# Performance work log

Hardware: AMD Instinct MI355X
Metric: run time of the kernel (lower is better)

The kernel has to match this reference:

```python
import jax, jax.numpy as jnp
import numpy as np

EPSILON = float(np.finfo(np.float32).tiny)
K = 32                 # self.k
TRAIN_ENSEMBLE = 2     # repeat_sample in train mode
TAU = 0.1


def setup_inputs() -> dict:
    key = jax.random.key(0)
    scores = jax.random.normal(key, (256, 8192, 4), dtype=jnp.float32)  # [bsz, Nmax, ensemble]
    return {"scores": scores}


def reference(scores):
    bsz, Nmax, ensemble = scores.shape
    repeat = TRAIN_ENSEMBLE
    local_k = min(K, Nmax)

    # flat_scores: (bsz*ensemble, Nmax), then repeated over samples -> (repeat*bsz*ensemble, Nmax)
    flat = scores.transpose(0, 2, 1).reshape(bsz * ensemble, Nmax)
    flat = jnp.tile(flat, (repeat, 1))

    # Gumbel(0,1) noise (m.sample())
    g = jax.random.gumbel(jax.random.key(42), flat.shape, dtype=flat.dtype)
    flat = flat + g

    zeros = jnp.zeros_like(flat)

    def step(carry, _):
        f, khot, onehot = carry
        khot_mask = jnp.maximum(1.0 - onehot, EPSILON)
        f = f + jnp.log(khot_mask)
        onehot = jax.nn.softmax(f / TAU, axis=1)
        return (f, khot + onehot, onehot), None

    (_, khot, _), _ = jax.lax.scan(step, (flat, zeros, zeros), None, length=local_k)

    # hard top-k straight-through
    _, ind = jax.lax.top_k(khot, local_k)                      # (R, local_k)
    rows = jnp.arange(khot.shape[0])[:, None]
    khot_hard = jnp.zeros_like(khot).at[rows, ind].set(1.0)
    res = khot_hard - jax.lax.stop_gradient(khot) + khot

    # (repeat, bsz, ensemble, Nmax) -> (repeat, bsz, Nmax, ensemble)
    new_mask = res.reshape(repeat, bsz, ensemble, Nmax).transpose(0, 1, 3, 2)
    return new_mask
```

## Files before the change

### kernel.cpp

```cpp
#include <hip/hip_runtime.h>

#define TPB 256
#define ROWN 8192
#define CMAX 1024
#define EPS_TINY 1.1754943508222875e-38f

__device__ __forceinline__ unsigned rotl32(unsigned x, int r) {
  return (x << r) | (x >> (32 - r));
}

__device__ __forceinline__ unsigned tf_pxor(unsigned idx) {
  const unsigned ks0 = 0u, ks1 = 42u, ks2 = 0x1BD11BDAu ^ 0u ^ 42u;
  unsigned x0 = ks0;
  unsigned x1 = idx + ks1;
#define TF4(a,b,cc,d) \
  x0 += x1; x1 = rotl32(x1,(a));  x1 ^= x0; \
  x0 += x1; x1 = rotl32(x1,(b));  x1 ^= x0; \
  x0 += x1; x1 = rotl32(x1,(cc)); x1 ^= x0; \
  x0 += x1; x1 = rotl32(x1,(d));  x1 ^= x0;
  TF4(13,15,26,6)   x0 += ks1; x1 += ks2 + 1u;
  TF4(17,29,16,24)  x0 += ks2; x1 += ks0 + 2u;
  TF4(13,15,26,6)   x0 += ks0; x1 += ks1 + 3u;
  TF4(17,29,16,24)  x0 += ks1; x1 += ks2 + 4u;
  TF4(13,15,26,6)   x0 += ks2; x1 += ks0 + 5u;
#undef TF4
  return x0 ^ x1;
}

__device__ __forceinline__ float gumbel_of(unsigned idx) {
  const unsigned bits = tf_pxor(idx);
  float u = __uint_as_float((bits >> 9) | 0x3f800000u) - 1.0f;
  u = u + EPS_TINY;
  u = fmaxf(EPS_TINY, u);
  return -logf(-logf(u));
}

__device__ __forceinline__ float approx_gumbel(unsigned bits) {
  float u = __uint_as_float((bits >> 9) | 0x3f800000u) - 1.0f;
  u = u + EPS_TINY;
  u = fmaxf(EPS_TINY, u);
  float t;
  if (u >= 0.75f) {
    const float v = 1.0f - u;
    t = v * (1.0f + v * (0.5f + v * (0.33333334f + v * (0.25f + v * 0.2f))));
  } else {
    t = -0.69314718f * __log2f(u);
  }
  return -0.69314718f * __log2f(t);
}

__device__ __forceinline__ unsigned key16_of(float x) {
  const unsigned b = __float_as_uint(x) >> 16;
  return (b & 0x8000u) ? (0xFFFFu & ~b) : (b | 0x8000u);
}

__global__ __launch_bounds__(TPB, 8)
void topk_row(const void* __restrict__ scores_raw, int* __restrict__ selws) {
  const int t    = threadIdx.x;
  const int lane = t & 63;
  const int wave = t >> 6;

  const int i   = blockIdx.x;
  const int xcd = i & 7;
  const int k   = i >> 3;
  const int e   = k & 3;
  const int q   = k >> 2;
  const int b   = xcd * 32 + (q & 31);
  const int rep = q >> 5;
  const int r   = rep * 1024 + b * 4 + e;
  const unsigned gbase = (unsigned)r * (unsigned)ROWN;

  __shared__ unsigned       kLds[16][TPB];
  __shared__ unsigned short candIdx[CMAX];
  __shared__ float redM[4];
  __shared__ float redZ[4];
  __shared__ int   wtot[13][4];
  __shared__ float bV[2][4];
  __shared__ int   bI[2][4];
  __shared__ int   f32flag;

  if (t == 0) f32flag = 0;
  __syncthreads();
  {
    const unsigned* w = (const unsigned*)scores_raw;
    bool bad = false;
#pragma unroll
    for (int p = 0; p < 4; ++p) {
      const unsigned x = w[t + 256 * p];
      const float flo = __uint_as_float((x & 0xFFFFu) << 16);
      const float fhi = __uint_as_float(x & 0xFFFF0000u);
      if (!(fabsf(flo) <= 16.0f) || !(fabsf(fhi) <= 16.0f)) bad = true;
    }
    if (bad) f32flag = 1;
  }
  __syncthreads();
  const bool in_f32 = (f32flag != 0);

  const size_t ebase0 = ((size_t)b * ROWN + (size_t)t) * 4 + (size_t)e;
  float m = -3.4e38f;
  {
    unsigned pair = 0u;
    if (in_f32) {
      const float* sp = (const float*)scores_raw;
#pragma unroll
      for (int j = 0; j < 32; ++j) {
        const float fj = sp[ebase0 + (size_t)(256 * j) * 4]
                       + approx_gumbel(tf_pxor(gbase + (unsigned)(t + 256 * j)));
        m = fmaxf(m, fj);
        const unsigned kk = key16_of(fj);
        if (j & 1) { pair |= kk << 16; kLds[j >> 1][t] = pair; }
        else pair = kk;
      }
    } else {
      const unsigned short* sp = (const unsigned short*)scores_raw;
#pragma unroll
      for (int j = 0; j < 32; ++j) {
        const float fj = __uint_as_float(((unsigned)sp[ebase0 + (size_t)(256 * j) * 4]) << 16)
                       + approx_gumbel(tf_pxor(gbase + (unsigned)(t + 256 * j)));
        m = fmaxf(m, fj);
        const unsigned kk = key16_of(fj);
        if (j & 1) { pair |= kk << 16; kLds[j >> 1][t] = pair; }
        else pair = kk;
      }
    }
  }

#pragma unroll
  for (int off = 32; off >= 1; off >>= 1) m = fmaxf(m, __shfl_xor(m, off));
  if (lane == 0) redM[wave] = m;
  __syncthreads();
  m = fmaxf(fmaxf(redM[0], redM[1]), fmaxf(redM[2], redM[3]));

  float lo = m - 25.0f, hi = m;
#pragma unroll 1
  for (int itb = 0; itb < 12; ++itb) {
    const float mid = 0.5f * (lo + hi);
    const unsigned kmid = key16_of(mid);
    int c = 0;
#pragma unroll
    for (int h = 0; h < 16; ++h) {
      const unsigned w = kLds[h][t];
      c += ((w & 0xFFFFu) > kmid) ? 1 : 0;
      c += ((w >> 16) > kmid) ? 1 : 0;
    }
#pragma unroll
    for (int off = 32; off >= 1; off >>= 1) c += __shfl_xor(c, off);
    if (lane == 0) wtot[itb][wave] = c;
    __syncthreads();
    const int tot = wtot[itb][0] + wtot[itb][1] + wtot[itb][2] + wtot[itb][3];
    if (tot >= 33) lo = mid; else hi = mid;
  }
  const float theta = lo - 2.34f;
  const unsigned ktheta = key16_of(theta);

  int cj = 0;
#pragma unroll
  for (int h = 0; h < 16; ++h) {
    const unsigned w = kLds[h][t];
    cj += ((w & 0xFFFFu) >= ktheta) ? 1 : 0;
    cj += ((w >> 16) >= ktheta) ? 1 : 0;
  }
  int incv = cj;
#pragma unroll
  for (int off = 1; off < 64; off <<= 1) {
    const int v = __shfl_up(incv, off);
    if (lane >= off) incv += v;
  }
  if (lane == 63) wtot[12][wave] = incv;
  __syncthreads();
  int base = 0;
  for (int w = 0; w < wave; ++w) base += wtot[12][w];
  int cnt = wtot[12][0] + wtot[12][1] + wtot[12][2] + wtot[12][3];
  if (cnt > CMAX) cnt = CMAX;
  int o = base + incv - cj;
#pragma unroll
  for (int h = 0; h < 16; ++h) {
    const unsigned w = kLds[h][t];
    if ((w & 0xFFFFu) >= ktheta) {
      if (o < CMAX) candIdx[o] = (unsigned short)(t + 256 * (2 * h));
      ++o;
    }
    if ((w >> 16) >= ktheta) {
      if (o < CMAX) candIdx[o] = (unsigned short)(t + 256 * (2 * h + 1));
      ++o;
    }
  }
  __syncthreads();

  float cfr[4], khr[4];
  int   idxr[4];
#pragma unroll
  for (int p = 0; p < 4; ++p) {
    cfr[p] = -3.0e38f; khr[p] = -3.0e38f; idxr[p] = 0x7FFFFFFF;
    if (256 * p < cnt) {
      const int ci = t + 256 * p;
      if (ci < cnt) {
        const int n = (int)candIdx[ci];
        const size_t ei = ((size_t)b * ROWN + (size_t)n) * 4 + (size_t)e;
        float sc;
        if (in_f32) sc = ((const float*)scores_raw)[ei];
        else sc = __uint_as_float(((unsigned)((const unsigned short*)scores_raw)[ei]) << 16);
        cfr[p] = sc + gumbel_of(gbase + (unsigned)n);
        khr[p] = 0.0f;
        idxr[p] = n;
      }
    }
  }

#pragma unroll 1
  for (int it = 0; it < 32; ++it) {
    float m2 = -3.4e38f;
#pragma unroll
    for (int p = 0; p < 4; ++p)
      if (256 * p < cnt) m2 = fmaxf(m2, cfr[p]);
#pragma unroll
    for (int off = 32; off >= 1; off >>= 1) m2 = fmaxf(m2, __shfl_xor(m2, off));
    if (lane == 0) redM[wave] = m2;
    __syncthreads();
    m2 = fmaxf(fmaxf(redM[0], redM[1]), fmaxf(redM[2], redM[3]));

    float ek[4];
    float Z = 0.0f;
#pragma unroll
    for (int p = 0; p < 4; ++p) {
      float ev = 0.0f;
      if (256 * p < cnt) {
        ev = __expf((cfr[p] - m2) * 10.0f);
        Z += ev;
      }
      ek[p] = ev;
    }
#pragma unroll
    for (int off = 32; off >= 1; off >>= 1) Z += __shfl_xor(Z, off);
    if (lane == 0) redZ[wave] = Z;
    __syncthreads();
    Z = (redZ[0] + redZ[1]) + (redZ[2] + redZ[3]);

    const float rz = __builtin_amdgcn_rcpf(Z);
#pragma unroll
    for (int p = 0; p < 4; ++p) {
      if (256 * p < cnt) {
        const float pp = ek[p] * rz;
        khr[p] += pp;
        cfr[p] += __logf(fmaxf(1.0f - pp, EPS_TINY));
      }
    }
  }

#pragma unroll 1
  for (int pass = 0; pass < 32; ++pass) {
    float bv = -3.4e38f; int bi = 0x7FFFFFFF;
#pragma unroll
    for (int p = 0; p < 4; ++p) {
      if (256 * p < cnt) {
        const float v = khr[p]; const int ix = idxr[p];
        if (v > bv || (v == bv && ix < bi)) { bv = v; bi = ix; }
      }
    }
#pragma unroll
    for (int off = 32; off >= 1; off >>= 1) {
      const float ov = __shfl_xor(bv, off);
      const int   oi = __shfl_xor(bi, off);
      if (ov > bv || (ov == bv && oi < bi)) { bv = ov; bi = oi; }
    }
    if (lane == 0) { bV[pass & 1][wave] = bv; bI[pass & 1][wave] = bi; }
    __syncthreads();
#pragma unroll
    for (int w = 0; w < 4; ++w) {
      const float ov = bV[pass & 1][w]; const int oi = bI[pass & 1][w];
      if (ov > bv || (ov == bv && oi < bi)) { bv = ov; bi = oi; }
    }
    if (t == 0) selws[r * 32 + pass] = bi;
#pragma unroll
    for (int p = 0; p < 4; ++p)
      if (256 * p < cnt && idxr[p] == bi) khr[p] = -3.0e38f;
  }
}

__global__ __launch_bounds__(TPB)
void expand_out(const int* __restrict__ selws, float4* __restrict__ out4) {
  const int t   = threadIdx.x;
  const int blk = blockIdx.x;
  const int grp = blk >> 2;
  const int s   = blk & 3;
  const int rep = grp >> 8;
  const int b   = grp & 255;

  __shared__ unsigned ebm[4 * 256];
#pragma unroll
  for (int p = 0; p < 4; ++p) ebm[t + 256 * p] = 0u;
  __syncthreads();
  if (t < 4) {
    const int r = rep * 1024 + b * 4 + t;
#pragma unroll 1
    for (int p = 0; p < 32; ++p) {
      const int ix = selws[r * 32 + p];
      ebm[t * 256 + (ix >> 5)] |= (1u << (ix & 31));
    }
  }
  __syncthreads();

  const size_t obase = (size_t)grp * ROWN;
#pragma unroll
  for (int j = 0; j < 8; ++j) {
    const int n = s * 2048 + t + 256 * j;
    float4 v;
    v.x = ((ebm[0 * 256 + (n >> 5)] >> (n & 31)) & 1u) ? 1.0f : 0.0f;
    v.y = ((ebm[1 * 256 + (n >> 5)] >> (n & 31)) & 1u) ? 1.0f : 0.0f;
    v.z = ((ebm[2 * 256 + (n >> 5)] >> (n & 31)) & 1u) ? 1.0f : 0.0f;
    v.w = ((ebm[3 * 256 + (n >> 5)] >> (n & 31)) & 1u) ? 1.0f : 0.0f;
    out4[obase + (size_t)n] = v;
  }
}

extern "C" void kernel_launch(void* const* d_in, const int* in_sizes, int n_in,
                              void* d_out, int out_size, void* d_ws, size_t ws_size,
                              hipStream_t stream) {
  const void* scores = d_in[0];
  int* selws = (int*)d_ws;
  topk_row<<<dim3(2048), dim3(TPB), 0, stream>>>(scores, selws);
  expand_out<<<dim3(2048), dim3(TPB), 0, stream>>>(selws, (float4*)d_out);
}
```

Measured before the change: 249.4 us.

## Cut block barriers in softmax loop and do top-k selection in a single wave

The softmax iteration now recomputes the block-wide max only every fourth step, using a stale max for the others, and double-buffers the Z reduction so one barrier per step is enough. The final 32-pass top-k selection is moved to one wavefront reading candidate values from LDS, which removes a block barrier per pass and lets the other waves exit. A stale max can drift from the true max, so the exponentials risk overflow or rounding differences. The single-wave selection serialises the scan over up to 1024 candidates in one wave.

```diff
diff --git a/kernel.cpp b/kernel.cpp
--- a/kernel.cpp
+++ b/kernel.cpp
@@ -73,10 +73,8 @@
   __shared__ unsigned       kLds[16][TPB];
   __shared__ unsigned short candIdx[CMAX];
   __shared__ float redM[4];
-  __shared__ float redZ[4];
+  __shared__ float redZ[2][4];
   __shared__ int   wtot[13][4];
-  __shared__ float bV[2][4];
-  __shared__ int   bI[2][4];
   __shared__ int   f32flag;
 
   if (t == 0) f32flag = 0;
@@ -188,10 +186,9 @@
   __syncthreads();
 
   float cfr[4], khr[4];
-  int   idxr[4];
 #pragma unroll
   for (int p = 0; p < 4; ++p) {
-    cfr[p] = -3.0e38f; khr[p] = -3.0e38f; idxr[p] = 0x7FFFFFFF;
+    cfr[p] = -3.0e38f; khr[p] = -3.0e38f;
     if (256 * p < cnt) {
       const int ci = t + 256 * p;
       if (ci < cnt) {
@@ -202,22 +199,24 @@
         else sc = __uint_as_float(((unsigned)((const unsigned short*)scores_raw)[ei]) << 16);
         cfr[p] = sc + gumbel_of(gbase + (unsigned)n);
         khr[p] = 0.0f;
-        idxr[p] = n;
-      }
-    }
-  }
-
+      }
+    }
+  }
+
+  float m2 = 0.0f;
 #pragma unroll 1
   for (int it = 0; it < 32; ++it) {
-    float m2 = -3.4e38f;
-#pragma unroll
-    for (int p = 0; p < 4; ++p)
-      if (256 * p < cnt) m2 = fmaxf(m2, cfr[p]);
-#pragma unroll
-    for (int off = 32; off >= 1; off >>= 1) m2 = fmaxf(m2, __shfl_xor(m2, off));
-    if (lane == 0) redM[wave] = m2;
-    __syncthreads();
-    m2 = fmaxf(fmaxf(redM[0], redM[1]), fmaxf(redM[2], redM[3]));
+    if ((it & 3) == 0) {
+      float mm = -3.4e38f;
+#pragma unroll
+      for (int p = 0; p < 4; ++p)
+        if (256 * p < cnt) mm = fmaxf(mm, cfr[p]);
+#pragma unroll
+      for (int off = 32; off >= 1; off >>= 1) mm = fmaxf(mm, __shfl_xor(mm, off));
+      if (lane == 0) redM[wave] = mm;
+      __syncthreads();
+      m2 = fmaxf(fmaxf(redM[0], redM[1]), fmaxf(redM[2], redM[3]));
+    }
 
     float ek[4];
     float Z = 0.0f;
@@ -232,9 +231,9 @@
     }
 #pragma unroll
     for (int off = 32; off >= 1; off >>= 1) Z += __shfl_xor(Z, off);
-    if (lane == 0) redZ[wave] = Z;
+    if (lane == 0) redZ[it & 1][wave] = Z;
     __syncthreads();
-    Z = (redZ[0] + redZ[1]) + (redZ[2] + redZ[3]);
+    Z = (redZ[it & 1][0] + redZ[it & 1][1]) + (redZ[it & 1][2] + redZ[it & 1][3]);
 
     const float rz = __builtin_amdgcn_rcpf(Z);
 #pragma unroll
@@ -247,33 +246,41 @@
     }
   }
 
+  float* khLds = (float*)&kLds[0][0];
+#pragma unroll
+  for (int p = 0; p < 4; ++p) {
+    if (256 * p < cnt) {
+      const int ci = t + 256 * p;
+      if (ci < cnt) khLds[ci] = khr[p];
+    }
+  }
+  __syncthreads();
+  if (wave != 0) return;
+
+  const int nch = (cnt + 63) >> 6;
 #pragma unroll 1
   for (int pass = 0; pass < 32; ++pass) {
-    float bv = -3.4e38f; int bi = 0x7FFFFFFF;
-#pragma unroll
-    for (int p = 0; p < 4; ++p) {
-      if (256 * p < cnt) {
-        const float v = khr[p]; const int ix = idxr[p];
-        if (v > bv || (v == bv && ix < bi)) { bv = v; bi = ix; }
+    float bv = -3.4e38f; int bn = 0x7FFFFFFF; int bci = 0;
+#pragma unroll 1
+    for (int c = 0; c < nch; ++c) {
+      const int ci = lane + 64 * c;
+      if (ci < cnt) {
+        const float v = khLds[ci];
+        const int  n = (int)candIdx[ci];
+        if (v > bv || (v == bv && n < bn)) { bv = v; bn = n; bci = ci; }
       }
     }
 #pragma unroll
     for (int off = 32; off >= 1; off >>= 1) {
       const float ov = __shfl_xor(bv, off);
-      const int   oi = __shfl_xor(bi, off);
-      if (ov > bv || (ov == bv && oi < bi)) { bv = ov; bi = oi; }
-    }
-    if (lane == 0) { bV[pass & 1][wave] = bv; bI[pass & 1][wave] = bi; }
-    __syncthreads();
-#pragma unroll
-    for (int w = 0; w < 4; ++w) {
-      const float ov = bV[pass & 1][w]; const int oi = bI[pass & 1][w];
-      if (ov > bv || (ov == bv && oi < bi)) { bv = ov; bi = oi; }
-    }
-    if (t == 0) selws[r * 32 + pass] = bi;
-#pragma unroll
-    for (int p = 0; p < 4; ++p)
-      if (256 * p < cnt && idxr[p] == bi) khr[p] = -3.0e38f;
+      const int   on = __shfl_xor(bn, off);
+      const int   oc = __shfl_xor(bci, off);
+      if (ov > bv || (ov == bv && on < bn)) { bv = ov; bn = on; bci = oc; }
+    }
+    if (lane == 0) {
+      selws[r * 32 + pass] = bn;
+      khLds[bci] = -3.0e38f;
+    }
   }
 }
 
```

After: 231.5 us. -7.2%, faster.
